# Performance work log

Hardware: AMD Instinct MI355X
Metric: run time of the kernel (lower is better)

## Reference

```python
import jax, jax.numpy as jnp
import numpy as np

N_NODES = 50000
N_EDGES = 600000
IN_DIM = 128
HID = 128
OUT_DIM = 10
N_GRAPHS = 512
LN_EPS = 1e-5
N_CELLS = 4  # len(macro_architecture) + 1


def setup_inputs() -> dict:
    key = jax.random.key(0)
    ks = jax.random.split(key, 8)
    s = 0.05
    x = jax.random.normal(ks[0], (N_NODES, IN_DIM), dtype=jnp.float32)
    edge_index = jax.random.randint(ks[1], (2, N_EDGES), 0, N_NODES, dtype=jnp.int32)
    batch = jnp.sort(jax.random.randint(ks[2], (N_NODES,), 0, N_GRAPHS, dtype=jnp.int32))
    return {
        "x": x,
        "edge_index": edge_index,
        "batch": batch,
        "W_pre": jax.random.normal(ks[3], (IN_DIM, HID), dtype=jnp.float32) * s,
        "b_pre": jnp.zeros((HID,), jnp.float32),
        "conv_W": jax.random.normal(ks[4], (N_CELLS, HID, HID), dtype=jnp.float32) * s,
        "conv_b": jnp.zeros((N_CELLS, HID), jnp.float32),
        "ln_g": jnp.ones((N_CELLS, HID), jnp.float32),
        "ln_b": jnp.zeros((N_CELLS, HID), jnp.float32),
        "W_post": jax.random.normal(ks[5], (HID, OUT_DIM), dtype=jnp.float32) * s,
        "b_post": jnp.zeros((OUT_DIM,), jnp.float32),
    }


def _gcn_conv(x, W, b, src, dst):
    """GCNConv: add self-loops, symmetric deg^-1/2 normalization, gather-scatter."""
    n = x.shape[0]
    h = x @ W                                   # [N, HID]
    loops = jnp.arange(n, dtype=src.dtype)
    s = jnp.concatenate([src, loops])           # [E + N]
    d = jnp.concatenate([dst, loops])
    deg = jax.ops.segment_sum(jnp.ones_like(d, jnp.float32), d, num_segments=n)
    dinv = jax.lax.rsqrt(jnp.maximum(deg, 1.0))  # deg >= 1 via self-loops
    coef = dinv[s] * dinv[d]                    # [E + N]
    out = jax.ops.segment_sum(h[s] * coef[:, None], d, num_segments=n)
    return out + b


def _layer_norm(x, g, b):
    mu = jnp.mean(x, axis=-1, keepdims=True)
    var = jnp.var(x, axis=-1, keepdims=True)
    return (x - mu) * jax.lax.rsqrt(var + LN_EPS) * g + b


def _cell(x, i, conv_W, conv_b, ln_g, ln_b, src, dst):
    h = _gcn_conv(x, conv_W[i], conv_b[i], src, dst)
    return jax.nn.relu(_layer_norm(h, ln_g[i], ln_b[i]))


def reference(x, edge_index, batch, W_pre, b_pre, conv_W, conv_b, ln_g, ln_b, W_post, b_post):
    src, dst = edge_index[0], edge_index[1]
    # pre MLP
    h0 = x @ W_pre + b_pre
    # state node 0 (all 3 outgoing edges active -> identical output reused)
    n0 = _cell(h0, 0, conv_W, conv_b, ln_g, ln_b, src, dst)
    # state node 1: input = node0's output
    n1 = _cell(n0, 1, conv_W, conv_b, ln_g, ln_b, src, dst)
    # second-to-last node: sum of [-2] outputs (n0, n1)
    s2l = _cell(n0 + n1, 2, conv_W, conv_b, ln_g, ln_b, src, dst)
    # last node: sum of [-1] outputs (n0, n1) + second-to-last output
    last = _cell(n0 + n1 + s2l, 3, conv_W, conv_b, ln_g, ln_b, src, dst)
    # sum pooling by graph id, then post MLP
    pooled = jax.ops.segment_sum(last, batch, num_segments=N_GRAPHS)  # [G, HID]
    return pooled @ W_post + b_post
```

## Files before the change

kernel.cpp:

```cpp
#include <hip/hip_runtime.h>

#define HID 128
#define LN_EPS 1e-5f

using f32x2 = __attribute__((ext_vector_type(2))) float;
using f32x4 = __attribute__((ext_vector_type(4))) float;
using s16x8 = __attribute__((ext_vector_type(8))) short;

__device__ inline float bl2f(unsigned u) { u <<= 16; return __builtin_bit_cast(float, u); }
__device__ inline float bh2f(unsigned u) { u &= 0xffff0000u; return __builtin_bit_cast(float, u); }
__device__ inline float sb2f(short s) {
  unsigned u = ((unsigned)(unsigned short)s) << 16;
  return __builtin_bit_cast(float, u);
}
__device__ inline unsigned f2b_bits(float f) {
  unsigned u = __builtin_bit_cast(unsigned, f);
  return (u + 0x7fffu + ((u >> 16) & 1u)) >> 16;
}
__device__ inline short f2b(float f) { return (short)f2b_bits(f); }
__device__ inline unsigned pack2(float a, float b) { return f2b_bits(a) | (f2b_bits(b) << 16); }
__device__ inline f32x2 up2(unsigned u) {
  f32x2 r; r.x = bl2f(u); r.y = bh2f(u); return r;
}


__global__ __launch_bounds__(64) void prep_w_kernel(const float* __restrict__ W_pre,
                                                    const float* __restrict__ conv_W,
                                                    short* __restrict__ Wt) {
  int b = blockIdx.x;
  int w = b >> 7, n = b & 127;
  const float* W = (w == 0) ? W_pre : conv_W + (size_t)(w - 1) * HID * HID;
  int t = threadIdx.x;
  float f0 = W[(2 * t) * HID + n];
  float f1 = W[(2 * t + 1) * HID + n];
  ((unsigned*)Wt)[(size_t)(w * HID + n) * 64 + t] = pack2(f0, f1);
}


__global__ void zero_ints_kernel(int* __restrict__ p, int n) {
  int i = blockIdx.x * blockDim.x + threadIdx.x;
  if (i < n) p[i] = 0;
}

__global__ void deg_count_kernel(const int* __restrict__ dst, int E, int* __restrict__ deg) {
  int e = blockIdx.x * blockDim.x + threadIdx.x;
  if (e < E) atomicAdd(&deg[dst[e]], 1);
}

__global__ __launch_bounds__(256) void alloc_kernel(const int* __restrict__ deg,
                                                    int* __restrict__ start,
                                                    int* __restrict__ cur,
                                                    float* __restrict__ dinv,
                                                    int* __restrict__ cnt, int n) {
  __shared__ int wt[4];
  __shared__ int bbase;
  int t = threadIdx.x, lane = t & 63, wid = t >> 6;
  int i = blockIdx.x * 256 + t;
  int d = (i < n) ? deg[i] : 0;
  int x = d;
  #pragma unroll
  for (int off = 1; off < 64; off <<= 1) {
    int u = __shfl_up(x, off, 64);
    if (lane >= off) x += u;
  }
  if (lane == 63) wt[wid] = x;
  __syncthreads();
  if (t == 0) bbase = atomicAdd(cnt, wt[0] + wt[1] + wt[2] + wt[3]);
  __syncthreads();
  int wbase = bbase;
  for (int w = 0; w < wid; ++w) wbase += wt[w];
  int excl = wbase + x - d;
  if (i < n) {
    start[i] = excl;
    cur[i] = excl;
    dinv[i] = rsqrtf((float)(d + 1));
  }
}

__global__ void fill_csr_kernel(const int* __restrict__ src, const int* __restrict__ dst,
                                int E, int* __restrict__ cur, int* __restrict__ col) {
  int e = blockIdx.x * blockDim.x + threadIdx.x;
  if (e < E) {
    int d = dst[e];
    int p = atomicAdd(&cur[d], 1);
    col[p] = src[e];
  }
}

#define HNODES 4096
__global__ __launch_bounds__(256) void hist_kernel(const int* __restrict__ deg,
                                                   int* __restrict__ hist, int n) {
  __shared__ int lh[64];
  int t = threadIdx.x;
  if (t < 64) lh[t] = 0;
  __syncthreads();
  int nend = min(n, (int)(blockIdx.x + 1) * HNODES);
  for (int i = blockIdx.x * HNODES + t; i < nend; i += 256)
    atomicAdd(&lh[min(deg[i], 63)], 1);
  __syncthreads();
  if (t < 64 && lh[t]) atomicAdd(&hist[t * 16], lh[t]);
}

__global__ __launch_bounds__(64) void binoff_kernel(const int* __restrict__ hist,
                                                    int* __restrict__ bincur) {
  int lane = threadIdx.x;
  int rb = 63 - lane;
  int v = hist[rb * 16];
  int x = v;
  #pragma unroll
  for (int off = 1; off < 64; off <<= 1) {
    int u = __shfl_up(x, off, 64);
    if (lane >= off) x += u;
  }
  bincur[rb * 16] = x - v;
}

#define SNODES 1024
__global__ __launch_bounds__(256) void scatter_kernel(const int* __restrict__ deg,
                                                      int* __restrict__ bincur,
                                                      int* __restrict__ perm, int n) {
  __shared__ int lh[64];
  __shared__ int lbase[64];
  int t = threadIdx.x;
  if (t < 64) lh[t] = 0;
  __syncthreads();
  int nstart = blockIdx.x * SNODES;
  int nend = min(n, nstart + SNODES);
  int myb[4], myrank[4];
  int cnt = 0;
  for (int i = nstart + t; i < nend; i += 256) {
    int b = min(deg[i], 63);
    myb[cnt] = b;
    myrank[cnt] = atomicAdd(&lh[b], 1);
    ++cnt;
  }
  __syncthreads();
  if (t < 64) lbase[t] = lh[t] ? atomicAdd(&bincur[t * 16], lh[t]) : 0;
  __syncthreads();
  int k = 0;
  for (int i = nstart + t; i < nend; i += 256, ++k)
    perm[lbase[myb[k]] + myrank[k]] = i;
}


__global__ __launch_bounds__(256) void gemm_mfma_kernel(
    const float* __restrict__ Xf, const short* __restrict__ Wt,
    const float* __restrict__ bias, const float* __restrict__ dinv,
    short* __restrict__ Y, int M) {
  __shared__ short lds[4 * 32 * HID];
  int t = threadIdx.x;
  int wave = t >> 6, l = t & 63;
  int lg = l >> 4, lr = l & 15;
  int mb = blockIdx.x * 128 + wave * 32;

  const f32x4 z4 = {0.f, 0.f, 0.f, 0.f};
  f32x4 acc[2][8];
  #pragma unroll
  for (int i = 0; i < 2; ++i)
    #pragma unroll
    for (int j = 0; j < 8; ++j) acc[i][j] = z4;

  #pragma unroll
  for (int kk = 0; kk < 4; ++kk) {
    int k0 = kk * 32 + lg * 8;
    s16x8 a[2];
    #pragma unroll
    for (int mf = 0; mf < 2; ++mf) {
      int row = mb + mf * 16 + lr;
      s16x8 av = {0, 0, 0, 0, 0, 0, 0, 0};
      if (row < M) {
        const float4* p = (const float4*)(Xf + (size_t)row * HID + k0);
        float4 x0 = p[0], x1 = p[1];
        av[0] = f2b(x0.x); av[1] = f2b(x0.y); av[2] = f2b(x0.z); av[3] = f2b(x0.w);
        av[4] = f2b(x1.x); av[5] = f2b(x1.y); av[6] = f2b(x1.z); av[7] = f2b(x1.w);
      }
      a[mf] = av;
    }
    #pragma unroll
    for (int nf = 0; nf < 8; ++nf) {
      s16x8 b = *(const s16x8*)(Wt + (size_t)(nf * 16 + lr) * HID + k0);
      acc[0][nf] = __builtin_amdgcn_mfma_f32_16x16x32_bf16(a[0], b, acc[0][nf], 0, 0, 0);
      acc[1][nf] = __builtin_amdgcn_mfma_f32_16x16x32_bf16(a[1], b, acc[1][nf], 0, 0, 0);
    }
  }

  float bv[8];
  #pragma unroll
  for (int nf = 0; nf < 8; ++nf) bv[nf] = bias[nf * 16 + lr];

  short* wsl = lds + wave * 32 * HID;
  #pragma unroll
  for (int mf = 0; mf < 2; ++mf) {
    #pragma unroll
    for (int r = 0; r < 4; ++r) {
      int ri = mf * 16 + lg * 4 + r;
      int row = mb + ri;
      float dv = (row < M) ? dinv[row] : 1.f;
      #pragma unroll
      for (int nf = 0; nf < 8; ++nf) {
        float v = (acc[mf][nf][r] + bv[nf]) * dv;
        wsl[ri * HID + nf * 16 + lr] = f2b(v);
      }
    }
  }
  __syncthreads();

  #pragma unroll
  for (int it = 0; it < 8; ++it) {
    int ro = it * 4 + lg;
    int row = mb + ro;
    s16x8 v = *(const s16x8*)(wsl + it * 512 + l * 8);
    if (row < M) *(s16x8*)(Y + (size_t)row * HID + lr * 8) = v;
  }
}


__global__ __launch_bounds__(512) void cell_kernel(
    const short* __restrict__ Sin, const int* __restrict__ start,
    const int* __restrict__ deg, const float* __restrict__ dinv,
    const int* __restrict__ col, const int* __restrict__ perm,
    const short* __restrict__ Wt, const float* __restrict__ bconv,
    const float* __restrict__ lng, const float* __restrict__ lnb,
    short* __restrict__ Sout, int N, int mode) {
  __shared__ short Zs[32 * HID];
  __shared__ float red[32][8][2];
  int t = threadIdx.x;
  int wave = t >> 6, l = t & 63, lr = l & 15, sub = l >> 4;
  const uint4* GR = (const uint4*)Sin;

  int rowL = wave * 4 + sub;
  int slot = blockIdx.x * 32 + rowL;
  int v = (slot < N) ? perm[slot] : -1;
  int zofs = rowL * HID + ((lr * 8) ^ ((rowL & 7) << 3));
  if (v >= 0) {
    uint4 us = GR[(size_t)v * 16 + lr];
    f32x2 a0 = up2(us.x), a1 = up2(us.y), a2 = up2(us.z), a3 = up2(us.w);
    int lo = start[v], hi = lo + deg[v];
    int j = lo;
    for (; j + 1 < hi; j += 2) {
      int c0 = col[j], c1 = col[j + 1];
      uint4 u0 = GR[(size_t)c0 * 16 + lr];
      uint4 u1 = GR[(size_t)c1 * 16 + lr];
      a0 += up2(u0.x); a1 += up2(u0.y); a2 += up2(u0.z); a3 += up2(u0.w);
      a0 += up2(u1.x); a1 += up2(u1.y); a2 += up2(u1.z); a3 += up2(u1.w);
    }
    if (j < hi) {
      uint4 u0 = GR[(size_t)col[j] * 16 + lr];
      a0 += up2(u0.x); a1 += up2(u0.y); a2 += up2(u0.z); a3 += up2(u0.w);
    }
    float d = dinv[v];
    uint4 q;
    q.x = pack2(a0.x * d, a0.y * d);
    q.y = pack2(a1.x * d, a1.y * d);
    q.z = pack2(a2.x * d, a2.y * d);
    q.w = pack2(a3.x * d, a3.y * d);
    *(uint4*)&Zs[zofs] = q;
  } else {
    *(uint4*)&Zs[zofs] = make_uint4(0u, 0u, 0u, 0u);
  }
  __syncthreads();

  f32x4 accA = {0.f, 0.f, 0.f, 0.f}, accB = {0.f, 0.f, 0.f, 0.f};
  #pragma unroll
  for (int kk = 0; kk < 4; ++kk) {
    int k0 = kk * 32 + sub * 8;
    s16x8 bf = *(const s16x8*)(Wt + (size_t)(wave * 16 + lr) * HID + k0);
    s16x8 afA = *(const s16x8*)&Zs[lr * HID + (k0 ^ ((lr & 7) << 3))];
    s16x8 afB = *(const s16x8*)&Zs[(16 + lr) * HID + (k0 ^ ((lr & 7) << 3))];
    accA = __builtin_amdgcn_mfma_f32_16x16x32_bf16(afA, bf, accA, 0, 0, 0);
    accB = __builtin_amdgcn_mfma_f32_16x16x32_bf16(afB, bf, accB, 0, 0, 0);
  }
  int c = wave * 16 + lr;
  float bc = bconv[c];
  float hA[4], hB[4], s1A[4], s2A[4], s1B[4], s2B[4];
  #pragma unroll
  for (int r = 0; r < 4; ++r) {
    hA[r] = accA[r] + bc; s1A[r] = hA[r]; s2A[r] = hA[r] * hA[r];
    hB[r] = accB[r] + bc; s1B[r] = hB[r]; s2B[r] = hB[r] * hB[r];
  }
  #pragma unroll
  for (int off = 1; off <= 8; off <<= 1) {
    #pragma unroll
    for (int r = 0; r < 4; ++r) {
      s1A[r] += __shfl_xor(s1A[r], off, 64);
      s2A[r] += __shfl_xor(s2A[r], off, 64);
      s1B[r] += __shfl_xor(s1B[r], off, 64);
      s2B[r] += __shfl_xor(s2B[r], off, 64);
    }
  }
  if (lr == 0) {
    #pragma unroll
    for (int r = 0; r < 4; ++r) {
      red[sub * 4 + r][wave][0] = s1A[r];
      red[sub * 4 + r][wave][1] = s2A[r];
      red[16 + sub * 4 + r][wave][0] = s1B[r];
      red[16 + sub * 4 + r][wave][1] = s2B[r];
    }
  }
  __syncthreads();
  float gl = lng[c], bl = lnb[c];
  #pragma unroll
  for (int r = 0; r < 4; ++r) {
    {
      int row = sub * 4 + r;
      const float4* rp = (const float4*)&red[row][0][0];
      float t1 = 0.f, t2 = 0.f;
      #pragma unroll
      for (int q4 = 0; q4 < 4; ++q4) { float4 vv = rp[q4]; t1 += vv.x + vv.z; t2 += vv.y + vv.w; }
      float mu = t1 * (1.f / HID);
      float var = t2 * (1.f / HID) - mu * mu;
      float inv = rsqrtf(fmaxf(var, 0.f) + LN_EPS);
      float yv = fmaxf(fmaf((hA[r] - mu) * inv, gl, bl), 0.f);
      Zs[row * HID + (c ^ ((row & 7) << 3))] = f2b(yv);
    }
    {
      int row = 16 + sub * 4 + r;
      const float4* rp = (const float4*)&red[row][0][0];
      float t1 = 0.f, t2 = 0.f;
      #pragma unroll
      for (int q4 = 0; q4 < 4; ++q4) { float4 vv = rp[q4]; t1 += vv.x + vv.z; t2 += vv.y + vv.w; }
      float mu = t1 * (1.f / HID);
      float var = t2 * (1.f / HID) - mu * mu;
      float inv = rsqrtf(fmaxf(var, 0.f) + LN_EPS);
      float yv = fmaxf(fmaf((hB[r] - mu) * inv, gl, bl), 0.f);
      Zs[row * HID + (c ^ ((row & 7) << 3))] = f2b(yv);
    }
  }
  __syncthreads();

  {
    int row = t >> 4, qq = t & 15;
    int slot2 = blockIdx.x * 32 + row;
    if (slot2 < N) {
      int v2 = perm[slot2];
      s16x8 y8 = *(const s16x8*)&Zs[row * HID + ((qq * 8) ^ ((row & 7) << 3))];
      float yv[8];
      #pragma unroll
      for (int i = 0; i < 8; ++i) yv[i] = sb2f(y8[i]);
      uint4 o;
      if (mode == 2) {
        o.x = pack2(yv[0], yv[1]); o.y = pack2(yv[2], yv[3]);
        o.z = pack2(yv[4], yv[5]); o.w = pack2(yv[6], yv[7]);
      } else if (mode == 0) {
        float d = dinv[v2];
        o.x = pack2(yv[0] * d, yv[1] * d); o.y = pack2(yv[2] * d, yv[3] * d);
        o.z = pack2(yv[4] * d, yv[5] * d); o.w = pack2(yv[6] * d, yv[7] * d);
      } else {
        float d = dinv[v2];
        uint4 ui = GR[(size_t)v2 * 16 + qq];
        o.x = pack2(bl2f(ui.x) + yv[0] * d, bh2f(ui.x) + yv[1] * d);
        o.y = pack2(bl2f(ui.y) + yv[2] * d, bh2f(ui.y) + yv[3] * d);
        o.z = pack2(bl2f(ui.z) + yv[4] * d, bh2f(ui.z) + yv[5] * d);
        o.w = pack2(bl2f(ui.w) + yv[6] * d, bh2f(ui.w) + yv[7] * d);
      }
      ((uint4*)Sout)[(size_t)v2 * 16 + qq] = o;
    }
  }
}


__device__ inline int lower_bound_i(const int* a, int n, int key) {
  int lo = 0, hi = n;
  while (lo < hi) { int m = (lo + hi) >> 1; if (a[m] < key) lo = m + 1; else hi = m; }
  return lo;
}

__global__ __launch_bounds__(128) void pool_post_kernel(
    const short* __restrict__ Yl, const int* __restrict__ batch, int n,
    const float* __restrict__ Wp, const float* __restrict__ bp,
    float* __restrict__ out, int n_out) {
  int g = blockIdx.x, t = threadIdx.x;
  int wave = t >> 6;
  int lr = t & 15, slot = t >> 4;
  int lo = lower_bound_i(batch, n, g);
  int hi = lower_bound_i(batch, n, g + 1);
  const uint4* YR = (const uint4*)Yl;
  float a[8] = {0.f, 0.f, 0.f, 0.f, 0.f, 0.f, 0.f, 0.f};
  for (int r = lo + slot; r < hi; r += 8) {
    uint4 u = YR[(size_t)r * 16 + lr];
    a[0] += bl2f(u.x); a[1] += bh2f(u.x);
    a[2] += bl2f(u.y); a[3] += bh2f(u.y);
    a[4] += bl2f(u.z); a[5] += bh2f(u.z);
    a[6] += bl2f(u.w); a[7] += bh2f(u.w);
  }
  #pragma unroll
  for (int i = 0; i < 8; ++i) {
    a[i] += __shfl_xor(a[i], 16, 64);
    a[i] += __shfl_xor(a[i], 32, 64);
  }
  __shared__ float ls[2][HID];
  if ((slot & 3) == 0) {
    #pragma unroll
    for (int i = 0; i < 8; ++i) ls[wave][8 * lr + i] = a[i];
  }
  __syncthreads();
  if (t < n_out) {
    float o = bp[t];
    #pragma unroll 8
    for (int k = 0; k < HID; ++k) o = fmaf(ls[0][k] + ls[1][k], Wp[k * n_out + t], o);
    out[g * n_out + t] = o;
  }
}


extern "C" void kernel_launch(void* const* d_in, const int* in_sizes, int n_in,
                              void* d_out, int out_size, void* d_ws, size_t ws_size,
                              hipStream_t stream) {
  const float* x      = (const float*)d_in[0];
  const int*   ei     = (const int*)d_in[1];
  const int*   batch  = (const int*)d_in[2];
  const float* W_pre  = (const float*)d_in[3];
  const float* b_pre  = (const float*)d_in[4];
  const float* conv_W = (const float*)d_in[5];
  const float* conv_b = (const float*)d_in[6];
  const float* ln_g   = (const float*)d_in[7];
  const float* ln_b   = (const float*)d_in[8];
  const float* W_post = (const float*)d_in[9];
  const float* b_post = (const float*)d_in[10];
  float* out = (float*)d_out;

  const int N = in_sizes[2];
  const int E = in_sizes[1] / 2;
  const int OUT_DIM = 10;
  const int NG = out_size / OUT_DIM;

  char* p = (char*)d_ws;
  short* SA  = (short*)p;            p += (size_t)N * HID * 2;
  short* SB  = (short*)p;            p += (size_t)N * HID * 2;
  short* Wt  = (short*)p;            p += (size_t)5 * HID * HID * 2;
  float* dinv = (float*)p;           p += (size_t)N * 4;
  int* deg   = (int*)p;              p += (size_t)(N + 1) * 4;
  int* startv = (int*)p;             p += (size_t)N * 4;
  int* cur   = (int*)p;              p += (size_t)N * 4;
  int* col   = (int*)p;              p += (size_t)E * 4;
  int* perm  = (int*)p;              p += (size_t)N * 4;
  int* hist  = (int*)p;              p += 64 * 16 * 4;
  int* bincur = (int*)p;             p += 64 * 16 * 4;
  int* cnt   = deg + N;

  const int* srcp = ei;
  const int* dstp = ei + E;

  int nb256 = (N + 255) / 256;
  int eb256 = (E + 255) / 256;
  int gemm_grid = (N + 127) / 128;
  int cell_grid = (N + 31) / 32;
  int hist_grid = (N + HNODES - 1) / HNODES;
  int scat_grid = (N + SNODES - 1) / SNODES;

  prep_w_kernel<<<5 * HID, 64, 0, stream>>>(W_pre, conv_W, Wt);

  zero_ints_kernel<<<nb256, 256, 0, stream>>>(deg, N + 1);
  zero_ints_kernel<<<4, 256, 0, stream>>>(hist, 64 * 16);
  deg_count_kernel<<<eb256, 256, 0, stream>>>(dstp, E, deg);
  alloc_kernel<<<nb256, 256, 0, stream>>>(deg, startv, cur, dinv, cnt, N);
  fill_csr_kernel<<<eb256, 256, 0, stream>>>(srcp, dstp, E, cur, col);
  hist_kernel<<<hist_grid, 256, 0, stream>>>(deg, hist, N);
  binoff_kernel<<<1, 64, 0, stream>>>(hist, bincur);
  scatter_kernel<<<scat_grid, 256, 0, stream>>>(deg, bincur, perm, N);

  gemm_mfma_kernel<<<gemm_grid, 256, 0, stream>>>(x, Wt + 0 * 16384, b_pre, dinv, SA, N);

  cell_kernel<<<cell_grid, 512, 0, stream>>>(SA, startv, deg, dinv, col, perm, Wt + 1 * 16384,
                                             conv_b + 0 * HID, ln_g + 0 * HID, ln_b + 0 * HID,
                                             SB, N, 0);
  cell_kernel<<<cell_grid, 512, 0, stream>>>(SB, startv, deg, dinv, col, perm, Wt + 2 * 16384,
                                             conv_b + 1 * HID, ln_g + 1 * HID, ln_b + 1 * HID,
                                             SA, N, 1);
  cell_kernel<<<cell_grid, 512, 0, stream>>>(SA, startv, deg, dinv, col, perm, Wt + 3 * 16384,
                                             conv_b + 2 * HID, ln_g + 2 * HID, ln_b + 2 * HID,
                                             SB, N, 1);
  cell_kernel<<<cell_grid, 512, 0, stream>>>(SB, startv, deg, dinv, col, perm, Wt + 4 * 16384,
                                             conv_b + 3 * HID, ln_g + 3 * HID, ln_b + 3 * HID,
                                             SA, N, 2);

  pool_post_kernel<<<NG, 128, 0, stream>>>(SA, batch, N, W_post, b_post, out, OUT_DIM);
}
```

Baseline: 273.0 us.

## Shrink cell blocks to 16 rows and unroll neighbor gather by four

The fused cell kernel now handles 16 nodes per block with 256 threads (4 waves) instead of 32 nodes with 512 threads. Each wave computes two 16-column MFMA tiles for one row tile rather than one column tile for two row tiles, and the LayerNorm reduction is regrouped to match. The neighbor aggregation loop is unrolled to four gathers per iteration to keep more memory loads in flight. The smaller blocks aim for better occupancy and load balance, at the cost of reading the weight matrix twice as often per node.

```diff
diff --git a/kernel.cpp b/kernel.cpp
--- a/kernel.cpp
+++ b/kernel.cpp
@@ -215,21 +215,21 @@
 }
 
 
-__global__ __launch_bounds__(512) void cell_kernel(
+__global__ __launch_bounds__(256, 8) void cell_kernel(
     const short* __restrict__ Sin, const int* __restrict__ start,
     const int* __restrict__ deg, const float* __restrict__ dinv,
     const int* __restrict__ col, const int* __restrict__ perm,
     const short* __restrict__ Wt, const float* __restrict__ bconv,
     const float* __restrict__ lng, const float* __restrict__ lnb,
     short* __restrict__ Sout, int N, int mode) {
-  __shared__ short Zs[32 * HID];
-  __shared__ float red[32][8][2];
+  __shared__ short Zs[16 * HID];
+  __shared__ float red[16][4][2];
   int t = threadIdx.x;
   int wave = t >> 6, l = t & 63, lr = l & 15, sub = l >> 4;
   const uint4* GR = (const uint4*)Sin;
 
   int rowL = wave * 4 + sub;
-  int slot = blockIdx.x * 32 + rowL;
+  int slot = blockIdx.x * 16 + rowL;
   int v = (slot < N) ? perm[slot] : -1;
   int zofs = rowL * HID + ((lr * 8) ^ ((rowL & 7) << 3));
   if (v >= 0) {
@@ -237,14 +237,18 @@
     f32x2 a0 = up2(us.x), a1 = up2(us.y), a2 = up2(us.z), a3 = up2(us.w);
     int lo = start[v], hi = lo + deg[v];
     int j = lo;
-    for (; j + 1 < hi; j += 2) {
-      int c0 = col[j], c1 = col[j + 1];
+    for (; j + 4 <= hi; j += 4) {
+      int c0 = col[j], c1 = col[j + 1], c2 = col[j + 2], c3 = col[j + 3];
       uint4 u0 = GR[(size_t)c0 * 16 + lr];
       uint4 u1 = GR[(size_t)c1 * 16 + lr];
-      a0 += up2(u0.x); a1 += up2(u0.y); a2 += up2(u0.z); a3 += up2(u0.w);
-      a0 += up2(u1.x); a1 += up2(u1.y); a2 += up2(u1.z); a3 += up2(u1.w);
-    }
-    if (j < hi) {
+      uint4 u2 = GR[(size_t)c2 * 16 + lr];
+      uint4 u3 = GR[(size_t)c3 * 16 + lr];
+      a0 += up2(u0.x) + up2(u1.x);  a1 += up2(u0.y) + up2(u1.y);
+      a2 += up2(u0.z) + up2(u1.z);  a3 += up2(u0.w) + up2(u1.w);
+      a0 += up2(u2.x) + up2(u3.x);  a1 += up2(u2.y) + up2(u3.y);
+      a2 += up2(u2.z) + up2(u3.z);  a3 += up2(u2.w) + up2(u3.w);
+    }
+    for (; j < hi; ++j) {
       uint4 u0 = GR[(size_t)col[j] * 16 + lr];
       a0 += up2(u0.x); a1 += up2(u0.y); a2 += up2(u0.z); a3 += up2(u0.w);
     }
@@ -260,77 +264,65 @@
   }
   __syncthreads();
 
-  f32x4 accA = {0.f, 0.f, 0.f, 0.f}, accB = {0.f, 0.f, 0.f, 0.f};
+  f32x4 acc0 = {0.f, 0.f, 0.f, 0.f}, acc1 = {0.f, 0.f, 0.f, 0.f};
+  int base = wave * 32;
   #pragma unroll
   for (int kk = 0; kk < 4; ++kk) {
     int k0 = kk * 32 + sub * 8;
-    s16x8 bf = *(const s16x8*)(Wt + (size_t)(wave * 16 + lr) * HID + k0);
-    s16x8 afA = *(const s16x8*)&Zs[lr * HID + (k0 ^ ((lr & 7) << 3))];
-    s16x8 afB = *(const s16x8*)&Zs[(16 + lr) * HID + (k0 ^ ((lr & 7) << 3))];
-    accA = __builtin_amdgcn_mfma_f32_16x16x32_bf16(afA, bf, accA, 0, 0, 0);
-    accB = __builtin_amdgcn_mfma_f32_16x16x32_bf16(afB, bf, accB, 0, 0, 0);
-  }
-  int c = wave * 16 + lr;
-  float bc = bconv[c];
-  float hA[4], hB[4], s1A[4], s2A[4], s1B[4], s2B[4];
+    s16x8 af = *(const s16x8*)&Zs[lr * HID + (k0 ^ ((lr & 7) << 3))];
+    s16x8 bf0 = *(const s16x8*)(Wt + (size_t)(base + lr) * HID + k0);
+    s16x8 bf1 = *(const s16x8*)(Wt + (size_t)(base + 16 + lr) * HID + k0);
+    acc0 = __builtin_amdgcn_mfma_f32_16x16x32_bf16(af, bf0, acc0, 0, 0, 0);
+    acc1 = __builtin_amdgcn_mfma_f32_16x16x32_bf16(af, bf1, acc1, 0, 0, 0);
+  }
+  int c0 = base + lr, c1 = base + 16 + lr;
+  float bc0 = bconv[c0], bc1 = bconv[c1];
+  float h0[4], h1[4], s1[4], s2[4];
   #pragma unroll
   for (int r = 0; r < 4; ++r) {
-    hA[r] = accA[r] + bc; s1A[r] = hA[r]; s2A[r] = hA[r] * hA[r];
-    hB[r] = accB[r] + bc; s1B[r] = hB[r]; s2B[r] = hB[r] * hB[r];
+    h0[r] = acc0[r] + bc0;
+    h1[r] = acc1[r] + bc1;
+    s1[r] = h0[r] + h1[r];
+    s2[r] = h0[r] * h0[r] + h1[r] * h1[r];
   }
   #pragma unroll
   for (int off = 1; off <= 8; off <<= 1) {
     #pragma unroll
     for (int r = 0; r < 4; ++r) {
-      s1A[r] += __shfl_xor(s1A[r], off, 64);
-      s2A[r] += __shfl_xor(s2A[r], off, 64);
-      s1B[r] += __shfl_xor(s1B[r], off, 64);
-      s2B[r] += __shfl_xor(s2B[r], off, 64);
+      s1[r] += __shfl_xor(s1[r], off, 64);
+      s2[r] += __shfl_xor(s2[r], off, 64);
     }
   }
   if (lr == 0) {
     #pragma unroll
     for (int r = 0; r < 4; ++r) {
-      red[sub * 4 + r][wave][0] = s1A[r];
-      red[sub * 4 + r][wave][1] = s2A[r];
-      red[16 + sub * 4 + r][wave][0] = s1B[r];
-      red[16 + sub * 4 + r][wave][1] = s2B[r];
-    }
-  }
-  __syncthreads();
-  float gl = lng[c], bl = lnb[c];
+      red[sub * 4 + r][wave][0] = s1[r];
+      red[sub * 4 + r][wave][1] = s2[r];
+    }
+  }
+  __syncthreads();
+  float gl0 = lng[c0], bl0 = lnb[c0], gl1 = lng[c1], bl1 = lnb[c1];
   #pragma unroll
   for (int r = 0; r < 4; ++r) {
-    {
-      int row = sub * 4 + r;
-      const float4* rp = (const float4*)&red[row][0][0];
-      float t1 = 0.f, t2 = 0.f;
-      #pragma unroll
-      for (int q4 = 0; q4 < 4; ++q4) { float4 vv = rp[q4]; t1 += vv.x + vv.z; t2 += vv.y + vv.w; }
-      float mu = t1 * (1.f / HID);
-      float var = t2 * (1.f / HID) - mu * mu;
-      float inv = rsqrtf(fmaxf(var, 0.f) + LN_EPS);
-      float yv = fmaxf(fmaf((hA[r] - mu) * inv, gl, bl), 0.f);
-      Zs[row * HID + (c ^ ((row & 7) << 3))] = f2b(yv);
-    }
-    {
-      int row = 16 + sub * 4 + r;
-      const float4* rp = (const float4*)&red[row][0][0];
-      float t1 = 0.f, t2 = 0.f;
-      #pragma unroll
-      for (int q4 = 0; q4 < 4; ++q4) { float4 vv = rp[q4]; t1 += vv.x + vv.z; t2 += vv.y + vv.w; }
-      float mu = t1 * (1.f / HID);
-      float var = t2 * (1.f / HID) - mu * mu;
-      float inv = rsqrtf(fmaxf(var, 0.f) + LN_EPS);
-      float yv = fmaxf(fmaf((hB[r] - mu) * inv, gl, bl), 0.f);
-      Zs[row * HID + (c ^ ((row & 7) << 3))] = f2b(yv);
-    }
+    int row = sub * 4 + r;
+    const float4* rp = (const float4*)&red[row][0][0];
+    float4 v0 = rp[0], v1 = rp[1];
+    float t1 = v0.x + v0.z + v1.x + v1.z;
+    float t2 = v0.y + v0.w + v1.y + v1.w;
+    float mu = t1 * (1.f / HID);
+    float var = t2 * (1.f / HID) - mu * mu;
+    float inv = rsqrtf(fmaxf(var, 0.f) + LN_EPS);
+    float yv0 = fmaxf(fmaf((h0[r] - mu) * inv, gl0, bl0), 0.f);
+    float yv1 = fmaxf(fmaf((h1[r] - mu) * inv, gl1, bl1), 0.f);
+    int sw = (row & 7) << 3;
+    Zs[row * HID + (c0 ^ sw)] = f2b(yv0);
+    Zs[row * HID + (c1 ^ sw)] = f2b(yv1);
   }
   __syncthreads();
 
   {
     int row = t >> 4, qq = t & 15;
-    int slot2 = blockIdx.x * 32 + row;
+    int slot2 = blockIdx.x * 16 + row;
     if (slot2 < N) {
       int v2 = perm[slot2];
       s16x8 y8 = *(const s16x8*)&Zs[row * HID + ((qq * 8) ^ ((row & 7) << 3))];
@@ -444,7 +436,7 @@
   int nb256 = (N + 255) / 256;
   int eb256 = (E + 255) / 256;
   int gemm_grid = (N + 127) / 128;
-  int cell_grid = (N + 31) / 32;
+  int cell_grid = (N + 15) / 16;
   int hist_grid = (N + HNODES - 1) / HNODES;
   int scat_grid = (N + SNODES - 1) / SNODES;
 
@@ -461,16 +453,16 @@
 
   gemm_mfma_kernel<<<gemm_grid, 256, 0, stream>>>(x, Wt + 0 * 16384, b_pre, dinv, SA, N);
 
-  cell_kernel<<<cell_grid, 512, 0, stream>>>(SA, startv, deg, dinv, col, perm, Wt + 1 * 16384,
+  cell_kernel<<<cell_grid, 256, 0, stream>>>(SA, startv, deg, dinv, col, perm, Wt + 1 * 16384,
                                              conv_b + 0 * HID, ln_g + 0 * HID, ln_b + 0 * HID,
                                              SB, N, 0);
-  cell_kernel<<<cell_grid, 512, 0, stream>>>(SB, startv, deg, dinv, col, perm, Wt + 2 * 16384,
+  cell_kernel<<<cell_grid, 256, 0, stream>>>(SB, startv, deg, dinv, col, perm, Wt + 2 * 16384,
                                              conv_b + 1 * HID, ln_g + 1 * HID, ln_b + 1 * HID,
                                              SA, N, 1);
-  cell_kernel<<<cell_grid, 512, 0, stream>>>(SA, startv, deg, dinv, col, perm, Wt + 3 * 16384,
+  cell_kernel<<<cell_grid, 256, 0, stream>>>(SA, startv, deg, dinv, col, perm, Wt + 3 * 16384,
                                              conv_b + 2 * HID, ln_g + 2 * HID, ln_b + 2 * HID,
                                              SB, N, 1);
-  cell_kernel<<<cell_grid, 512, 0, stream>>>(SB, startv, deg, dinv, col, perm, Wt + 4 * 16384,
+  cell_kernel<<<cell_grid, 256, 0, stream>>>(SB, startv, deg, dinv, col, perm, Wt + 4 * 16384,
                                              conv_b + 3 * HID, ln_g + 3 * HID, ln_b + 3 * HID,
                                              SA, N, 2);
 
```

Result: no change. 269.6 us (-1.3%).
